# Kernel optimization log

Hardware: AMD Instinct MI355X
Metric: run time of the kernel (lower is better)

Reference implementation:

```python
import jax, jax.numpy as jnp
import numpy as np

NUM_HEADS = 12
NUM_GROUPS = 4
LN_EPS = 1e-12
NEG = -10000.0


def _ln(x, g, b):
    m = x.mean(-1, keepdims=True)
    v = ((x - m) ** 2).mean(-1, keepdims=True)
    return (x - m) * jax.lax.rsqrt(v + LN_EPS) * g + b


def _attention(h, ext_mask, Wattn, battn, ln):
    # h: [B,S,H]; ext_mask additive [B,1,1,S]; Wattn [4,H,H] = (q,k,v,o); battn [4,H]; ln [2,H]
    B, S, H = h.shape
    dh = H // NUM_HEADS
    q = (h @ Wattn[0] + battn[0]).reshape(B, S, NUM_HEADS, dh)
    k = (h @ Wattn[1] + battn[1]).reshape(B, S, NUM_HEADS, dh)
    v = (h @ Wattn[2] + battn[2]).reshape(B, S, NUM_HEADS, dh)
    scores = jnp.einsum('bqhd,bkhd->bhqk', q, k) * (1.0 / np.sqrt(dh)) + ext_mask
    p = jax.nn.softmax(scores, axis=-1)
    ctx = jnp.einsum('bhqk,bkhd->bqhd', p, v).reshape(B, S, H)
    # BertSelfOutput: dense + residual + LayerNorm
    return _ln(ctx @ Wattn[3] + battn[3] + h, ln[0], ln[1])


def _ffn(x, Wi, bi, Wo, bo, ln):
    # BertIntermediate (gelu) + BertOutput (dense + residual + LayerNorm)
    return _ln(jax.nn.gelu(x @ Wi + bi, approximate=False) @ Wo + bo + x, ln[0], ln[1])


def _bert_layer(h, ext_mask, Wattn, battn, ln_attn, Wi, bi, Wo, bo, ln_out):
    a = _attention(h, ext_mask, Wattn, battn, ln_attn)
    return _ffn(a, Wi, bi, Wo, bo, ln_out)


def _hier_attention(h, hier_mask, Wattn, battn, ln_attn, Wi, bi, Wo, bo, ln_out):
    # group masks [G,B,S]: 1 where hier_mask == group_id (ids 1..G)
    gids = jnp.arange(1, NUM_GROUPS + 1)
    masks = (hier_mask[None] == gids[:, None, None]).astype(h.dtype)  # [G,B,S]
    ext = (1.0 - masks)[:, :, None, None, :] * NEG                    # [G,B,1,1,S]
    # one full BertLayer per group (vectorized over G instead of batch concat)
    outs = jax.vmap(lambda m: _bert_layer(h, m, Wattn, battn, ln_attn, Wi, bi, Wo, bo, ln_out))(ext)  # [G,B,S,H]
    return jnp.sum(outs * masks[..., None], axis=0)


def reference(hidden_states, attention_mask, main_Wattn, main_battn, main_ln_attn,
              main_Wi, main_bi, main_Wo, main_bo, main_ln_out,
              hier_Wattn, hier_battn, hier_ln_attn, hier_Wi, hier_bi, hier_Wo,
              hier_bo, hier_ln_out, hier_mask):
    attn_out = _attention(hidden_states, attention_mask, main_Wattn, main_battn, main_ln_attn)
    hier_out = _hier_attention(hidden_states, hier_mask, hier_Wattn, hier_battn,
                               hier_ln_attn, hier_Wi, hier_bi, hier_Wo, hier_bo, hier_ln_out)
    combined = attn_out + hier_out
    return _ffn(combined, main_Wi, main_bi, main_Wo, main_bo, main_ln_out)


def setup_inputs() -> dict:
    key = jax.random.key(0)
    ks = jax.random.split(key, 20)
    B, S, H, F = 8, 512, 768, 3072
    W = 0.02  # weight init scale

    def layer_params(k):
        kk = jax.random.split(k, 8)
        return dict(
            Wattn=jax.random.normal(kk[0], (4, H, H), jnp.float32) * W,
            battn=jax.random.normal(kk[1], (4, H), jnp.float32) * W,
            ln_attn=jnp.stack([1.0 + jax.random.normal(kk[2], (H,), jnp.float32) * W,
                               jax.random.normal(kk[3], (H,), jnp.float32) * W]),
            Wi=jax.random.normal(kk[4], (H, F), jnp.float32) * W,
            bi=jax.random.normal(kk[5], (F,), jnp.float32) * W,
            Wo=jax.random.normal(kk[6], (F, H), jnp.float32) * W,
            bo=jax.random.normal(kk[7], (H,), jnp.float32) * W,
            ln_out=jnp.stack([1.0 + jax.random.normal(kk[2], (H,), jnp.float32) * W,
                              jax.random.normal(kk[3], (H,), jnp.float32) * W]),
        )

    main = layer_params(ks[0])
    hier = layer_params(ks[1])
    inp = {
        'hidden_states': jax.random.normal(ks[2], (B, S, H), jnp.float32),
        'attention_mask': jnp.zeros((B, 1, 1, S), jnp.float32),
        'hier_mask': jax.random.randint(ks[3], (B, S), 0, 5).astype(jnp.int64),
    }
    for name, p in (('main', main), ('hier', hier)):
        for k2, v in p.items():
            inp[f'{name}_{k2}'] = v
    return inp
```

## Files before the change

kernel.cpp:

```cpp
#include <hip/hip_runtime.h>
#include <hip/hip_bf16.h>

#define DI __device__ __forceinline__

typedef __attribute__((ext_vector_type(4))) float  f32x4;
typedef __attribute__((ext_vector_type(8))) short  s16x8;
typedef __attribute__((ext_vector_type(4))) short  s16x4;
typedef __attribute__((ext_vector_type(8))) __bf16 bf16x8;

DI short f2bf(float f) {
  union { float f; unsigned u; } v; v.f = f;
  unsigned r = v.u + 0x7fffu + ((v.u >> 16) & 1u);
  return (short)(r >> 16);
}

DI f32x4 mfma16(s16x8 a, s16x8 b, f32x4 c) {
  return __builtin_amdgcn_mfma_f32_16x16x32_bf16(
      __builtin_bit_cast(bf16x8, a), __builtin_bit_cast(bf16x8, b), c, 0, 0, 0);
}

typedef const __attribute__((address_space(1))) unsigned* gas_p;
typedef __attribute__((address_space(3))) unsigned* las_p;
DI void gload16(const void* g, void* l) {
  __builtin_amdgcn_global_load_lds((gas_p)g, (las_p)l, 16, 0, 0);
}

template<int N> DI void wait_vmcnt() {
  asm volatile("s_waitcnt vmcnt(%0)" :: "n"(N) : "memory");
}

__global__ __launch_bounds__(256) void cast_bf16(const float* __restrict__ x,
                                                 short* __restrict__ y) {
  const int i = (blockIdx.x * 256 + threadIdx.x) * 4;
  const float4 t = *(const float4*)&x[i];
  s16x4 o;
  o[0] = f2bf(t.x); o[1] = f2bf(t.y); o[2] = f2bf(t.z); o[3] = f2bf(t.w);
  *(s16x4*)&y[i] = o;
}

struct TJob { const float* src; short* dst; int K, N, tile0; };
struct TJobs { TJob j[12]; };

__global__ __launch_bounds__(256) void transpose_w(TJobs jobs) {
  __shared__ float T[32][33];
  const int t = blockIdx.x;
  int ji = 0;
#pragma unroll
  for (int i = 1; i < 12; ++i) if (jobs.j[i].tile0 <= t) ji = i;
  const float* src = jobs.j[ji].src;
  short* dst = jobs.j[ji].dst;
  const int K = jobs.j[ji].K, N = jobs.j[ji].N;
  const int lt = t - jobs.j[ji].tile0;
  const int tn = N >> 5;
  const int n0 = (lt % tn) << 5, k0 = (lt / tn) << 5;
  const int tid = threadIdx.x;
#pragma unroll
  for (int i = 0; i < 4; ++i) {
    const int c = i * 256 + tid, r = c >> 5, cc = c & 31;
    T[cc][r] = src[(long long)(k0 + r) * N + n0 + cc];
  }
  __syncthreads();
#pragma unroll
  for (int i = 0; i < 4; ++i) {
    const int c = i * 256 + tid, r = c >> 5, cc = c & 31;
    dst[(long long)(n0 + r) * K + k0 + cc] = f2bf(T[r][cc]);
  }
}

__global__ __launch_bounds__(256) void transpose_v(const short* __restrict__ QKV,
                                                   short* __restrict__ Vt) {
  __shared__ short T[64][72];
  const int bh = blockIdx.y;
  const int b = bh / 12, hh = bh % 12;
  const int s0 = blockIdx.x * 64;
  const int tid = threadIdx.x;
#pragma unroll
  for (int i = 0; i < 2; ++i) {
    const int c = i * 256 + tid;
    const int s = c >> 3, d = (c & 7) * 8;
    s16x8 v = *(const s16x8*)&QKV[(long long)(b * 512 + s0 + s) * 2304 + 1536 + hh * 64 + d];
    *(s16x8*)&T[s][d] = v;
  }
  __syncthreads();
#pragma unroll
  for (int i = 0; i < 2; ++i) {
    const int c = i * 256 + tid;
    const int d = c >> 3, s = (c & 7) * 8;
    s16x8 v;
#pragma unroll
    for (int j = 0; j < 8; ++j) v[j] = T[s + j][d];
    *(s16x8*)&Vt[(long long)bh * 32768 + (long long)d * 512 + s0 + s] = v;
  }
}

template<int BM, int BN, int WM, int WN, int EPI>
__global__ __launch_bounds__(256) void gemm_bt(
    const short* __restrict__ A, int lda, long long sA,
    const short* __restrict__ B, int ldb, long long sB,
    void* __restrict__ Cv, int ldc,
    long long cOuter, int cInner, int cStride,
    const float* __restrict__ bias,
    int K, int nSplit) {
  constexpr int BK = 32;
  constexpr int WNW = BN / WN;
  constexpr int MFR = WM / 16, NFR = WN / 16;
  constexpr int ALD = BM / 64;
  constexpr int BLD = BN / 64;
  constexpr int LPT = ALD + BLD;

  __shared__ short As[3][BM * BK];
  __shared__ short Bs[3][BN * BK];

  const int z = blockIdx.z;
  const int zb = z / nSplit, zs = z - zb * nSplit;
  const short* Ab = A + (long long)zb * sA + (long long)zs * K;
  const short* Bb = B + (long long)zb * sB + (long long)zs * K;
  const long long cOff = (long long)(z / cInner) * cOuter + (long long)(z % cInner) * cStride;

  const int bm = blockIdx.x * BM;
  const int bn = blockIdx.y * BN;
  const int tid = threadIdx.x;
  const int wave = tid >> 6, lane = tid & 63;
  const int wm = (wave / WNW) * WM;
  const int wn = (wave % WNW) * WN;
  const int l16 = lane & 15, lk = lane >> 4;

  const int scol = ((tid & 3) ^ ((tid >> 3) & 3)) * 8;
  const short* aBase = Ab + (long long)(bm + (tid >> 2)) * lda + scol;
  const short* bBase = Bb + (long long)(bn + (tid >> 2)) * ldb + scol;
  const int ldsOff = wave * 64 * 8;

  const int rslot = (lk ^ ((l16 >> 1) & 3)) * 8;

  f32x4 acc[MFR][NFR] = {};

  auto stage = [&](int buf, int kt) {
#pragma unroll
    for (int i = 0; i < ALD; ++i)
      gload16(aBase + kt + (long long)(i * 64) * lda, &As[buf][i * 2048 + ldsOff]);
#pragma unroll
    for (int i = 0; i < BLD; ++i)
      gload16(bBase + kt + (long long)(i * 64) * ldb, &Bs[buf][i * 2048 + ldsOff]);
  };

  const int nt = K / BK;
  stage(0, 0);
  if (nt > 1) stage(1, BK);
  int cur = 0;
  for (int t = 0; t < nt; ++t) {
    if (t + 1 < nt) wait_vmcnt<LPT>();
    else            wait_vmcnt<0>();
    __builtin_amdgcn_s_barrier();
    s16x8 af[MFR], bfr[NFR];
#pragma unroll
    for (int mi = 0; mi < MFR; ++mi)
      af[mi] = *(const s16x8*)&As[cur][(wm + mi * 16 + l16) * BK + rslot];
#pragma unroll
    for (int ni = 0; ni < NFR; ++ni)
      bfr[ni] = *(const s16x8*)&Bs[cur][(wn + ni * 16 + l16) * BK + rslot];
#pragma unroll
    for (int mi = 0; mi < MFR; ++mi)
#pragma unroll
      for (int ni = 0; ni < NFR; ++ni)
        acc[mi][ni] = mfma16(bfr[ni], af[mi], acc[mi][ni]);
    if (t + 2 < nt) {
      const int nb = cur + 2 >= 3 ? cur - 1 : cur + 2;
      stage(nb, (t + 2) * BK);
    }
    cur = (cur + 1 == 3) ? 0 : cur + 1;
  }

#pragma unroll
  for (int mi = 0; mi < MFR; ++mi) {
    const int row = bm + wm + mi * 16 + l16;
#pragma unroll
    for (int ni = 0; ni < NFR; ++ni) {
      const int col = bn + wn + ni * 16 + lk * 4;
      const long long idx = cOff + (long long)row * ldc + col;
      f32x4 bv = {};
      if (EPI != 2 && bias) bv = *(const f32x4*)&bias[col];
      f32x4 v = acc[mi][ni] + bv;
      if constexpr (EPI == 0) {
        s16x4 o;
#pragma unroll
        for (int r = 0; r < 4; ++r) o[r] = f2bf(v[r]);
        *(s16x4*)&((short*)Cv)[idx] = o;
      } else if constexpr (EPI == 1) {
        s16x4 o;
#pragma unroll
        for (int r = 0; r < 4; ++r) {
          const float g = 0.5f * v[r] * (1.f + erff(v[r] * 0.70710678118654752f));
          o[r] = f2bf(g);
        }
        *(s16x4*)&((short*)Cv)[idx] = o;
      } else {
        *(f32x4*)&((float*)Cv)[idx] = v;
      }
    }
  }
}

template<int HIER>
__global__ __launch_bounds__(256) void attn_scores(
    const short* __restrict__ QKV,
    const float* __restrict__ amask,
    const int* __restrict__ hmask,
    short* __restrict__ P) {
  __shared__ short Qs[32 * 64];
  __shared__ short Ks[256 * 64];
  __shared__ float red[32 * 4];
  __shared__ int   hm[512];

  const int bh = blockIdx.y;
  const int b = bh / 12, hh = bh % 12;
  const int q0 = blockIdx.x * 32;
  const int tid = threadIdx.x;
  const int wave = tid >> 6, lane = tid & 63;
  const int l16 = lane & 15, lk = lane >> 4;
  const long long rowbase = (long long)(b * 512) * 2304 + hh * 64;

  {
    const int c = tid;
    const int d8 = ((c & 7) ^ ((c >> 3) & 7)) * 8;
    gload16(QKV + rowbase + (long long)(q0 + (c >> 3)) * 2304 + d8,
            &Qs[wave * 64 * 8]);
  }
  if constexpr (HIER) {
    for (int i = tid; i < 512; i += 256) hm[i] = hmask[b * 512 + i];
  }

  f32x4 acc[2][8] = {};
#pragma unroll
  for (int kc = 0; kc < 2; ++kc) {
    if (kc) __syncthreads();
#pragma unroll
    for (int i = 0; i < 8; ++i) {
      const int c = i * 256 + tid;
      const int d8 = ((c & 7) ^ ((c >> 3) & 7)) * 8;
      gload16(QKV + rowbase + 768 + (long long)(kc * 256 + (c >> 3)) * 2304 + d8,
              &Ks[(i * 256 + wave * 64) * 8]);
    }
    __syncthreads();
#pragma unroll
    for (int ks = 0; ks < 2; ++ks) {
      s16x8 af[2], bfr[4];
#pragma unroll
      for (int mi = 0; mi < 2; ++mi)
        af[mi] = *(const s16x8*)&Qs[(mi * 16 + l16) * 64 +
                                    (((ks * 4 + lk) ^ (l16 & 7)) * 8)];
#pragma unroll
      for (int ni = 0; ni < 4; ++ni)
        bfr[ni] = *(const s16x8*)&Ks[(wave * 64 + ni * 16 + l16) * 64 +
                                     (((ks * 4 + lk) ^ (l16 & 7)) * 8)];
#pragma unroll
      for (int mi = 0; mi < 2; ++mi)
#pragma unroll
        for (int ni = 0; ni < 4; ++ni)
          acc[mi][kc * 4 + ni] = mfma16(af[mi], bfr[ni], acc[mi][kc * 4 + ni]);
    }
  }

  int gq[2][4];
  if constexpr (HIER) {
#pragma unroll
    for (int mi = 0; mi < 2; ++mi)
#pragma unroll
      for (int r = 0; r < 4; ++r)
        gq[mi][r] = hm[q0 + mi * 16 + lk * 4 + r];
  }
  int hk[8]; float am[8];
#pragma unroll
  for (int nig = 0; nig < 8; ++nig) {
    const int col = (nig >> 2) * 256 + wave * 64 + (nig & 3) * 16 + l16;
    if constexpr (HIER) hk[nig] = hm[col];
    else                am[nig] = amask[b * 512 + col];
  }
#pragma unroll
  for (int mi = 0; mi < 2; ++mi)
#pragma unroll
    for (int nig = 0; nig < 8; ++nig)
#pragma unroll
      for (int r = 0; r < 4; ++r) {
        float v = acc[mi][nig][r] * 0.125f;
        if constexpr (HIER) v += (hk[nig] == gq[mi][r]) ? 0.f : -10000.f;
        else                v += am[nig];
        acc[mi][nig][r] = v;
      }

  float mx[2][4];
#pragma unroll
  for (int mi = 0; mi < 2; ++mi)
#pragma unroll
    for (int r = 0; r < 4; ++r) {
      float m = acc[mi][0][r];
#pragma unroll
      for (int nig = 1; nig < 8; ++nig) m = fmaxf(m, acc[mi][nig][r]);
#pragma unroll
      for (int d = 1; d < 16; d <<= 1) m = fmaxf(m, __shfl_xor(m, d));
      mx[mi][r] = m;
      red[(mi * 16 + lk * 4 + r) * 4 + wave] = m;
    }
  __syncthreads();
#pragma unroll
  for (int mi = 0; mi < 2; ++mi)
#pragma unroll
    for (int r = 0; r < 4; ++r) {
      const int q = mi * 16 + lk * 4 + r;
      mx[mi][r] = fmaxf(fmaxf(red[q * 4], red[q * 4 + 1]),
                        fmaxf(red[q * 4 + 2], red[q * 4 + 3]));
    }
  __syncthreads();

  float sm[2][4];
#pragma unroll
  for (int mi = 0; mi < 2; ++mi)
#pragma unroll
    for (int r = 0; r < 4; ++r) {
      float s = 0.f;
#pragma unroll
      for (int nig = 0; nig < 8; ++nig) {
        const float e = __expf(acc[mi][nig][r] - mx[mi][r]);
        acc[mi][nig][r] = e;
        s += e;
      }
#pragma unroll
      for (int d = 1; d < 16; d <<= 1) s += __shfl_xor(s, d);
      sm[mi][r] = s;
      red[(mi * 16 + lk * 4 + r) * 4 + wave] = s;
    }
  __syncthreads();
#pragma unroll
  for (int mi = 0; mi < 2; ++mi)
#pragma unroll
    for (int r = 0; r < 4; ++r) {
      const int q = mi * 16 + lk * 4 + r;
      sm[mi][r] = 1.f / (red[q * 4] + red[q * 4 + 1] + red[q * 4 + 2] + red[q * 4 + 3]);
    }

  const long long Pbase = (long long)bh * 512 * 512;
#pragma unroll
  for (int mi = 0; mi < 2; ++mi)
#pragma unroll
    for (int nig = 0; nig < 8; ++nig) {
      const int col = (nig >> 2) * 256 + wave * 64 + (nig & 3) * 16 + l16;
#pragma unroll
      for (int r = 0; r < 4; ++r) {
        const int q = mi * 16 + lk * 4 + r;
        P[Pbase + (long long)(q0 + q) * 512 + col] = f2bf(acc[mi][nig][r] * sm[mi][r]);
      }
    }
}

template<int NS, int MODE>
__global__ __launch_bounds__(256) void ln_red(
    const float* __restrict__ part, const float* __restrict__ bias,
    const float* __restrict__ res, const float* __restrict__ ln,
    float* __restrict__ outf, short* __restrict__ outb,
    const int* __restrict__ hmask) {
  constexpr long long SP = 4096LL * 768;
  const int row = blockIdx.x * 4 + (threadIdx.x >> 6);
  const int lane = threadIdx.x & 63;
  const long long rb = (long long)row * 768;
  float v[12];
  float s = 0.f;
#pragma unroll
  for (int i = 0; i < 3; ++i) {
    const int c4 = lane + (i << 6);
    float4 t = ((const float4*)(res + rb))[c4];
    const float4 bv = ((const float4*)bias)[c4];
    t.x += bv.x; t.y += bv.y; t.z += bv.z; t.w += bv.w;
#pragma unroll
    for (int ss = 0; ss < NS; ++ss) {
      const float4 p = ((const float4*)(part + ss * SP + rb))[c4];
      t.x += p.x; t.y += p.y; t.z += p.z; t.w += p.w;
    }
    v[i * 4 + 0] = t.x; v[i * 4 + 1] = t.y; v[i * 4 + 2] = t.z; v[i * 4 + 3] = t.w;
    s += t.x + t.y + t.z + t.w;
  }
#pragma unroll
  for (int d = 1; d < 64; d <<= 1) s += __shfl_xor(s, d);
  const float mean = s * (1.f / 768.f);
  float vs = 0.f;
#pragma unroll
  for (int i = 0; i < 12; ++i) { const float dv = v[i] - mean; vs += dv * dv; }
#pragma unroll
  for (int d = 1; d < 64; d <<= 1) vs += __shfl_xor(vs, d);
  const float rstd = rsqrtf(vs * (1.f / 768.f) + 1e-12f);
  int keep = 1;
  if constexpr (MODE == 2) keep = (hmask[row] != 0);
#pragma unroll
  for (int i = 0; i < 3; ++i) {
    const int c4 = lane + (i << 6);
    const float4 g = ((const float4*)ln)[c4];
    const float4 be = ((const float4*)(ln + 768))[c4];
    const float gg[4] = {g.x, g.y, g.z, g.w}, bb[4] = {be.x, be.y, be.z, be.w};
    float resv[4];
#pragma unroll
    for (int j = 0; j < 4; ++j) {
      float yv = (v[i * 4 + j] - mean) * rstd * gg[j] + bb[j];
      if constexpr (MODE == 2) {
        const float a = outf[rb + c4 * 4 + j];
        yv = a + (keep ? yv : 0.f);
      }
      resv[j] = yv;
    }
    float4 of; of.x = resv[0]; of.y = resv[1]; of.z = resv[2]; of.w = resv[3];
    ((float4*)(outf + rb))[c4] = of;
    if constexpr (MODE >= 1) {
      s16x4 ob;
#pragma unroll
      for (int j = 0; j < 4; ++j) ob[j] = f2bf(resv[j]);
      *(s16x4*)&outb[rb + c4 * 4] = ob;
    }
  }
}

extern "C" void kernel_launch(void* const* d_in, const int* in_sizes, int n_in,
                              void* d_out, int out_size, void* d_ws, size_t ws_size,
                              hipStream_t stream) {
  (void)in_sizes; (void)n_in; (void)out_size; (void)ws_size;
  const float* h      = (const float*)d_in[0];
  const float* amask  = (const float*)d_in[1];
  const int*   hmask  = (const int*)d_in[2];
  const float* mWattn = (const float*)d_in[3];
  const float* mbattn = (const float*)d_in[4];
  const float* mlnA   = (const float*)d_in[5];
  const float* mWi    = (const float*)d_in[6];
  const float* mbi    = (const float*)d_in[7];
  const float* mWo    = (const float*)d_in[8];
  const float* mbo    = (const float*)d_in[9];
  const float* mlnO   = (const float*)d_in[10];
  const float* hWattn = (const float*)d_in[11];
  const float* hbattn = (const float*)d_in[12];
  const float* hlnA   = (const float*)d_in[13];
  const float* hWi    = (const float*)d_in[14];
  const float* hbi    = (const float*)d_in[15];
  const float* hWo    = (const float*)d_in[16];
  const float* hbo    = (const float*)d_in[17];
  const float* hlnO   = (const float*)d_in[18];
  float* out = (float*)d_out;

  char* ws = (char*)d_ws;
  size_t off = 0;
  auto alloc = [&](size_t bytes) {
    void* p = ws + off;
    off += (bytes + 255) & ~(size_t)255;
    return p;
  };
  short* wq_m = (short*)alloc(2304ull * 768 * 2);
  short* wq_h = (short*)alloc(2304ull * 768 * 2);
  short* wo2  = (short*)alloc(2ull * 768 * 768 * 2);
  short* wi_m = (short*)alloc(3072ull * 768 * 2);
  short* wi_h = (short*)alloc(3072ull * 768 * 2);
  short* wf_m = (short*)alloc(768ull * 3072 * 2);
  short* wf_h = (short*)alloc(768ull * 3072 * 2);
  short* hbf  = (short*)alloc(4096ull * 768 * 2);
  short* qkv  = (short*)alloc(4096ull * 2304 * 2);
  short* vt   = (short*)alloc(96ull * 64 * 512 * 2);
  short* Pb   = (short*)alloc(96ull * 512 * 512 * 2);
  short* ctxb = (short*)alloc(2ull * 4096 * 768 * 2);
  float* pre1 = (float*)alloc(4096ull * 768 * 4);
  float* attn = (float*)alloc(4096ull * 768 * 4);
  short* abf  = (short*)alloc(4096ull * 768 * 2);
  short* cbf  = (short*)alloc(4096ull * 768 * 2);
  short* mid  = qkv;
  float* part = (float*)Pb;

  const long long SC = 4096LL * 768;

  cast_bf16<<<dim3(3072), dim3(256), 0, stream>>>(h, hbf);

  TJobs tj; int tile = 0; int nj = 0;
  auto add = [&](const float* s, short* d, int K, int N) {
    tj.j[nj].src = s; tj.j[nj].dst = d; tj.j[nj].K = K; tj.j[nj].N = N; tj.j[nj].tile0 = tile;
    tile += (K / 32) * (N / 32); nj++;
  };
  add(mWattn,              wq_m,              768, 768);
  add(mWattn + 589824,     wq_m + 589824,     768, 768);
  add(mWattn + 2 * 589824, wq_m + 2 * 589824, 768, 768);
  add(mWattn + 3 * 589824, wo2,               768, 768);
  add(mWi,                 wi_m,              768, 3072);
  add(mWo,                 wf_m,              3072, 768);
  add(hWattn,              wq_h,              768, 768);
  add(hWattn + 589824,     wq_h + 589824,     768, 768);
  add(hWattn + 2 * 589824, wq_h + 2 * 589824, 768, 768);
  add(hWattn + 3 * 589824, wo2 + 589824,      768, 768);
  add(hWi,                 wi_h,              768, 3072);
  add(hWo,                 wf_h,              3072, 768);
  transpose_w<<<dim3(tile), dim3(256), 0, stream>>>(tj);

  auto attn_path = [&](const short* wq, const float* battn, int hier, short* ctx) {
    gemm_bt<128, 128, 64, 64, 0><<<dim3(32, 18, 1), dim3(256), 0, stream>>>(
        hbf, 768, 0, wq, 768, 0, qkv, 2304, 0, 1, 0, battn, 768, 1);
    transpose_v<<<dim3(8, 96), dim3(256), 0, stream>>>(qkv, vt);
    if (hier)
      attn_scores<1><<<dim3(16, 96), dim3(256), 0, stream>>>(qkv, amask, hmask, Pb);
    else
      attn_scores<0><<<dim3(16, 96), dim3(256), 0, stream>>>(qkv, amask, hmask, Pb);
    gemm_bt<128, 64, 32, 64, 0><<<dim3(4, 1, 96), dim3(256), 0, stream>>>(
        Pb, 512, 262144LL, vt, 512, 32768LL,
        ctx, 768, 512LL * 768, 12, 64, nullptr, 512, 1);
  };

  attn_path(wq_m, mbattn, 0, ctxb);
  attn_path(wq_h, hbattn, 1, ctxb + SC);

  gemm_bt<128, 128, 64, 64, 2><<<dim3(32, 6, 4), dim3(256), 0, stream>>>(
      ctxb, 768, SC, wo2, 768, 589824LL, part, 768, SC, 1, 0, nullptr, 384, 2);
  ln_red<2, 0><<<dim3(1024), dim3(256), 0, stream>>>(
      part, mbattn + 2304, h, mlnA, attn, nullptr, nullptr);
  ln_red<2, 1><<<dim3(1024), dim3(256), 0, stream>>>(
      part + 2 * SC, hbattn + 2304, h, hlnA, pre1, abf, nullptr);

  gemm_bt<128, 128, 64, 64, 1><<<dim3(32, 24, 1), dim3(256), 0, stream>>>(
      abf, 768, 0, wi_h, 768, 0, mid, 3072, 0, 1, 0, hbi, 768, 1);
  gemm_bt<128, 128, 64, 64, 2><<<dim3(32, 6, 4), dim3(256), 0, stream>>>(
      mid, 3072, 0, wf_h, 3072, 0, part, 768, SC, 1, 0, nullptr, 768, 4);
  ln_red<4, 2><<<dim3(1024), dim3(256), 0, stream>>>(
      part, hbo, pre1, hlnO, attn, cbf, hmask);

  gemm_bt<128, 128, 64, 64, 1><<<dim3(32, 24, 1), dim3(256), 0, stream>>>(
      cbf, 768, 0, wi_m, 768, 0, mid, 3072, 0, 1, 0, mbi, 768, 1);
  gemm_bt<128, 128, 64, 64, 2><<<dim3(32, 6, 4), dim3(256), 0, stream>>>(
      mid, 3072, 0, wf_m, 3072, 0, part, 768, SC, 1, 0, nullptr, 768, 4);
  ln_red<4, 0><<<dim3(1024), dim3(256), 0, stream>>>(
      part, mbo, attn, mlnO, out, nullptr, nullptr);
}
```

Before: 375.8 us.

## Add 256x256 tile GEMM with 8 waves and triple buffering for FFN

Adds a new gemm256 kernel that uses 256x256 output tiles, 512 threads (8 waves each owning a 128x64 sub-tile), and a three-stage LDS ring buffer with BK=32. The four FFN GEMMs (intermediate with GELU and split-K output projection) now use it instead of the 128x128 gemm_bt. Larger tiles raise arithmetic intensity and cut global and LDS traffic per FLOP. In exchange, far fewer blocks are launched (192 per GEMM), which may underfill the GPU's compute units, and each wave holds 32 accumulator fragments, which raises register pressure.

```diff
diff --git a/kernel.cpp b/kernel.cpp
--- a/kernel.cpp
+++ b/kernel.cpp
@@ -129,7 +129,6 @@
   const short* aBase = Ab + (long long)(bm + (tid >> 2)) * lda + scol;
   const short* bBase = Bb + (long long)(bn + (tid >> 2)) * ldb + scol;
   const int ldsOff = wave * 64 * 8;
-
   const int rslot = (lk ^ ((l16 >> 1) & 3)) * 8;
 
   f32x4 acc[MFR][NFR] = {};
@@ -186,6 +185,101 @@
         for (int r = 0; r < 4; ++r) o[r] = f2bf(v[r]);
         *(s16x4*)&((short*)Cv)[idx] = o;
       } else if constexpr (EPI == 1) {
+        s16x4 o;
+#pragma unroll
+        for (int r = 0; r < 4; ++r) {
+          const float g = 0.5f * v[r] * (1.f + erff(v[r] * 0.70710678118654752f));
+          o[r] = f2bf(g);
+        }
+        *(s16x4*)&((short*)Cv)[idx] = o;
+      } else {
+        *(f32x4*)&((float*)Cv)[idx] = v;
+      }
+    }
+  }
+}
+
+template<int EPI>
+__global__ __launch_bounds__(512, 2) void gemm256(
+    const short* __restrict__ A, int lda,
+    const short* __restrict__ B, int ldb,
+    void* __restrict__ Cv, int ldc, long long cOuter,
+    const float* __restrict__ bias,
+    int K) {
+  constexpr int BK = 32;
+  constexpr int LPT = 4;
+
+  __shared__ short As[3][256 * BK];
+  __shared__ short Bs[3][256 * BK];
+
+  const int zs = blockIdx.z;
+  const short* Ab = A + (long long)zs * K;
+  const short* Bb = B + (long long)zs * K;
+  const long long cOff = (long long)zs * cOuter;
+
+  const int bm = blockIdx.x * 256;
+  const int bn = blockIdx.y * 256;
+  const int tid = threadIdx.x;
+  const int wave = tid >> 6, lane = tid & 63;
+  const int wm = (wave >> 2) * 128;
+  const int wn = (wave & 3) * 64;
+  const int l16 = lane & 15, lk = lane >> 4;
+
+  const int scol = ((tid & 3) ^ ((tid >> 3) & 3)) * 8;
+  const short* aBase = Ab + (long long)(bm + (tid >> 2)) * lda + scol;
+  const short* bBase = Bb + (long long)(bn + (tid >> 2)) * ldb + scol;
+  const int ldsOff = wave * 512;
+  const int rslot = (lk ^ ((l16 >> 1) & 3)) * 8;
+
+  f32x4 acc[8][4] = {};
+
+  auto stage = [&](int buf, int kt) {
+#pragma unroll
+    for (int i = 0; i < 2; ++i)
+      gload16(aBase + kt + (long long)(i * 128) * lda, &As[buf][i * 4096 + ldsOff]);
+#pragma unroll
+    for (int i = 0; i < 2; ++i)
+      gload16(bBase + kt + (long long)(i * 128) * ldb, &Bs[buf][i * 4096 + ldsOff]);
+  };
+
+  const int nt = K / BK;
+  stage(0, 0);
+  if (nt > 1) stage(1, BK);
+  int cur = 0;
+  for (int t = 0; t < nt; ++t) {
+    if (t + 1 < nt) wait_vmcnt<LPT>();
+    else            wait_vmcnt<0>();
+    __builtin_amdgcn_s_barrier();
+    s16x8 af[8], bfr[4];
+#pragma unroll
+    for (int mi = 0; mi < 8; ++mi)
+      af[mi] = *(const s16x8*)&As[cur][(wm + mi * 16 + l16) * BK + rslot];
+#pragma unroll
+    for (int ni = 0; ni < 4; ++ni)
+      bfr[ni] = *(const s16x8*)&Bs[cur][(wn + ni * 16 + l16) * BK + rslot];
+#pragma unroll
+    for (int mi = 0; mi < 8; ++mi)
+#pragma unroll
+      for (int ni = 0; ni < 4; ++ni)
+        acc[mi][ni] = mfma16(bfr[ni], af[mi], acc[mi][ni]);
+    if (t + 2 < nt) {
+      const int nb = cur + 2 >= 3 ? cur - 1 : cur + 2;
+      stage(nb, (t + 2) * BK);
+    }
+    cur = (cur + 1 == 3) ? 0 : cur + 1;
+  }
+
+#pragma unroll
+  for (int mi = 0; mi < 8; ++mi) {
+    const int row = bm + wm + mi * 16 + l16;
+#pragma unroll
+    for (int ni = 0; ni < 4; ++ni) {
+      const int col = bn + wn + ni * 16 + lk * 4;
+      const long long idx = cOff + (long long)row * ldc + col;
+      f32x4 bv = {};
+      if (EPI != 2 && bias) bv = *(const f32x4*)&bias[col];
+      f32x4 v = acc[mi][ni] + bv;
+      if constexpr (EPI == 1) {
         s16x4 o;
 #pragma unroll
         for (int r = 0; r < 4; ++r) {
@@ -512,17 +606,17 @@
   ln_red<2, 1><<<dim3(1024), dim3(256), 0, stream>>>(
       part + 2 * SC, hbattn + 2304, h, hlnA, pre1, abf, nullptr);
 
-  gemm_bt<128, 128, 64, 64, 1><<<dim3(32, 24, 1), dim3(256), 0, stream>>>(
-      abf, 768, 0, wi_h, 768, 0, mid, 3072, 0, 1, 0, hbi, 768, 1);
-  gemm_bt<128, 128, 64, 64, 2><<<dim3(32, 6, 4), dim3(256), 0, stream>>>(
-      mid, 3072, 0, wf_h, 3072, 0, part, 768, SC, 1, 0, nullptr, 768, 4);
+  gemm256<1><<<dim3(16, 12, 1), dim3(512), 0, stream>>>(
+      abf, 768, wi_h, 768, mid, 3072, 0, hbi, 768);
+  gemm256<2><<<dim3(16, 3, 4), dim3(512), 0, stream>>>(
+      mid, 3072, wf_h, 3072, part, 768, SC, nullptr, 768);
   ln_red<4, 2><<<dim3(1024), dim3(256), 0, stream>>>(
       part, hbo, pre1, hlnO, attn, cbf, hmask);
 
-  gemm_bt<128, 128, 64, 64, 1><<<dim3(32, 24, 1), dim3(256), 0, stream>>>(
-      cbf, 768, 0, wi_m, 768, 0, mid, 3072, 0, 1, 0, mbi, 768, 1);
-  gemm_bt<128, 128, 64, 64, 2><<<dim3(32, 6, 4), dim3(256), 0, stream>>>(
-      mid, 3072, 0, wf_m, 3072, 0, part, 768, SC, 1, 0, nullptr, 768, 4);
+  gemm256<1><<<dim3(16, 12, 1), dim3(512), 0, stream>>>(
+      cbf, 768, wi_m, 768, mid, 3072, 0, mbi, 768);
+  gemm256<2><<<dim3(16, 3, 4), dim3(512), 0, stream>>>(
+      mid, 3072, wf_m, 3072, part, 768, SC, nullptr, 768);
   ln_red<4, 0><<<dim3(1024), dim3(256), 0, stream>>>(
       part, mbo, attn, mlnO, out, nullptr, nullptr);
 }
```

After: 398.3 us. 6.0% more time.
